# Kernel tuning notes

Hardware: AMD Instinct MI355X
Metric: run time of the kernel (lower is better)

The kernel has to match this reference:

```python
import jax, jax.numpy as jnp
import numpy as np

B, S, E, H, D = 2, 2048, 1024, 16, 64


def setup_inputs() -> dict:
    key = jax.random.key(0)
    ks = jax.random.split(key, 6)
    hidden_states = jax.random.normal(ks[0], (B, S, E), dtype=jnp.float32)
    # causal mask over (SeqLen, KeySeqLen): 1 = attend, 0 = blocked
    mask = jnp.tril(jnp.ones((S, S), dtype=jnp.float32))
    W_attn = jax.random.normal(ks[1], (E, 3, H, D), dtype=jnp.float32) * (E ** -0.5)
    b_attn = jnp.zeros((3, H, D), dtype=jnp.float32)
    W_proj = jax.random.normal(ks[2], (H, D, E), dtype=jnp.float32) * (E ** -0.5)
    b_proj = jnp.zeros((E,), dtype=jnp.float32)
    W_v_ff = jax.random.normal(ks[3], (E, E), dtype=jnp.float32) * (E ** -0.5)
    W_v_gate = jax.random.normal(ks[4], (E, E), dtype=jnp.float32) * (E ** -0.5)
    return {
        "hidden_states": hidden_states,
        "mask": mask,
        "layer_idx": 3,
        "W_attn": W_attn,
        "b_attn": b_attn,
        "W_proj": W_proj,
        "b_proj": b_proj,
        "W_v_ff": W_v_ff,
        "W_v_gate": W_v_gate,
    }


def reference(hidden_states, mask, layer_idx, W_attn, b_attn, W_proj, b_proj, W_v_ff, W_v_gate):
    dtype = hidden_states.dtype
    # c_attn: [B,S,E] -> [B,3,S,H,D]
    qkv = jnp.einsum("bse,eqhd->bqshd", hidden_states, W_attn) + b_attn[:, None, :, :]
    q, k, v = qkv[:, 0], qkv[:, 1], qkv[:, 2]  # [B,S,H,D] (k,v use key-seq axis)

    scale = jax.lax.rsqrt(float(D)) / (layer_idx + 1.0)  # scale_by_inverse_layer_idx
    q = q * scale
    # upcast to fp32 for score computation
    q32 = q.astype(jnp.float32)
    k32 = k.astype(jnp.float32)

    # attention scores: [B,H,S,Skv]
    scores = jnp.einsum("bshd,bthd->bhst", q32, k32)
    scores = scores + (1.0 - mask) * -1e9
    attn_weights = jax.nn.softmax(scores, axis=-1).astype(dtype)
    # dropout is identity (inference=True / p=0)

    # gated V FFN applied over the flattened (H,D) == Embed axis of v
    v_flat = v.reshape(B, S, E)
    v_gate = v_flat @ W_v_gate
    v_ff = v_flat @ W_v_ff
    v_gated = (jax.nn.relu(v_gate) * v_ff).reshape(B, S, H, D)

    # weighted sum over KeySeqLen: [B,S,H,D]
    attn_output = jnp.einsum("bhst,bthd->bshd", attn_weights, v_gated)
    # c_proj: [B,S,H,D] -> [B,S,E]
    out = jnp.einsum("bshd,hde->bse", attn_output, W_proj) + b_proj
    return out
```

## Files before the change

### kernel.cpp

```cpp
#include <hip/hip_runtime.h>
#include <hip/hip_bf16.h>
#include <cstdint>
#include <cstddef>

typedef unsigned short u16;
typedef __bf16 bf16x8 __attribute__((ext_vector_type(8)));
typedef float f32x4 __attribute__((ext_vector_type(4)));

#define LOG2E 1.44269504088896340736f

__device__ __forceinline__ uint32_t f2bf2(float lo, float hi) {
  uint32_t r;
  asm("v_cvt_pk_bf16_f32 %0, %1, %2" : "=v"(r) : "v"(lo), "v"(hi));
  return r;
}
__device__ __forceinline__ u16 f2bf(float f) { return (u16)f2bf2(f, f); }

__device__ __forceinline__ void gload16(const u16* g, u16* l) {
  __builtin_amdgcn_global_load_lds(
      (const __attribute__((address_space(1))) void*)g,
      (__attribute__((address_space(3))) void*)l, 16, 0, 0);
}

__device__ __forceinline__ void xcd_swizzle(int& bx, int& by) {
  const int gx = gridDim.x;
  const int nwg = gx * gridDim.y;
  const int bid = blockIdx.y * gx + blockIdx.x;
  const int s = (bid & 7) * (nwg >> 3) + (bid >> 3);
  bx = s % gx;
  by = s / gx;
}

__global__ __launch_bounds__(256) void transpose_bf16_kernel(
    const float* __restrict__ src, u16* __restrict__ dst, int ld, int c0) {
  __shared__ u16 tile[64][65];
  const int r0 = blockIdx.x * 64, cl0 = blockIdx.y * 64;
  const int tid = threadIdx.x;
#pragma unroll
  for (int i = 0; i < 16; ++i) {
    int idx = i * 256 + tid;
    int r = idx >> 6, c = idx & 63;
    tile[c][r] = f2bf(src[(size_t)(r0 + r) * ld + c0 + cl0 + c]);
  }
  __syncthreads();
#pragma unroll
  for (int i = 0; i < 16; ++i) {
    int idx = i * 256 + tid;
    int c = idx >> 6, r = idx & 63;
    dst[(size_t)(cl0 + c) * 1024 + r0 + r] = tile[c][r];
  }
}

__global__ __launch_bounds__(256) void prep3_kernel(
    const float* __restrict__ Wa, const float* __restrict__ Wg,
    const float* __restrict__ Wf,
    u16* __restrict__ dv, u16* __restrict__ dg, u16* __restrict__ df) {
  __shared__ u16 tile[64][65];
  const int z = blockIdx.z;
  const float* src = (z == 0) ? Wa : (z == 1) ? Wg : Wf;
  u16* dst = (z == 0) ? dv : (z == 1) ? dg : df;
  const int ld = (z == 0) ? 3072 : 1024;
  const int c0 = (z == 0) ? 2048 : 0;
  const int r0 = blockIdx.x * 64, cl0 = blockIdx.y * 64;
  const int tid = threadIdx.x;
#pragma unroll
  for (int i = 0; i < 16; ++i) {
    int idx = i * 256 + tid;
    int r = idx >> 6, c = idx & 63;
    tile[c][r] = f2bf(src[(size_t)(r0 + r) * ld + c0 + cl0 + c]);
  }
  __syncthreads();
#pragma unroll
  for (int i = 0; i < 16; ++i) {
    int idx = i * 256 + tid;
    int c = idx >> 6, r = idx & 63;
    dst[(size_t)(cl0 + c) * 1024 + r0 + r] = tile[c][r];
  }
}

template <int EPI>
__global__ __launch_bounds__(256) void gemm_hA(
    const float* __restrict__ A,
    const u16* __restrict__ Bt,
    u16* __restrict__ O0, u16* __restrict__ O1,
    const float* __restrict__ bias,
    const int* __restrict__ layer_idx) {
  __shared__ u16 lds_a[2][64 * 40];
  __shared__ u16 lds_b[2][128 * 32];
  const int tid = threadIdx.x;
  const int wid = tid >> 6, lane = tid & 63;
  const int lrow = lane & 15, lgrp = lane >> 4;
  int bxs, bys;
  xcd_swizzle(bxs, bys);
  const int brow = bys * 64;
  const int bcol = bxs * 128;
  const int wr = wid >> 1, wc = wid & 1;

  f32x4 acc[2][4] = {};

  const int wchunk0 = wid, wchunk1 = 4 + wid;
  const int cB0 = wchunk0 * 64 + lane, cB1 = wchunk1 * 64 + lane;
  const int rB0 = cB0 >> 2, col8B0 = (cB0 & 3) << 3;
  const int rB1 = cB1 >> 2, col8B1 = (cB1 & 3) << 3;

  gload16(Bt + (size_t)(bcol + rB0) * 1024 + col8B0, lds_b[0] + wchunk0 * 512);
  gload16(Bt + (size_t)(bcol + rB1) * 1024 + col8B1, lds_b[0] + wchunk1 * 512);
  {
    float4 v[2];
#pragma unroll
    for (int j = 0; j < 2; ++j) {
      int idx = j * 256 + tid;
      int m = idx >> 3, k4 = (idx & 7) << 2;
      v[j] = *(const float4*)(A + (size_t)(brow + m) * 1024 + k4);
    }
#pragma unroll
    for (int j = 0; j < 2; ++j) {
      int idx = j * 256 + tid;
      int m = idx >> 3, k4 = (idx & 7) << 2;
      uint2 w;
      w.x = f2bf2(v[j].x, v[j].y);
      w.y = f2bf2(v[j].z, v[j].w);
      *(uint2*)(lds_a[0] + m * 40 + k4) = w;
    }
  }

  for (int k0 = 0; k0 < 1024; k0 += 32) {
    const int bi = (k0 >> 5) & 1;
    __syncthreads();
    bf16x8 af[2], bfr[4];
#pragma unroll
    for (int mi = 0; mi < 2; ++mi)
      af[mi] = *(const bf16x8*)(lds_a[bi] + (wr * 32 + mi * 16 + lrow) * 40 + lgrp * 8);
#pragma unroll
    for (int nj = 0; nj < 4; ++nj)
      bfr[nj] = *(const bf16x8*)(lds_b[bi] + (wc * 64 + nj * 16 + lrow) * 32 + lgrp * 8);

    float4 v[2];
    if (k0 < 992) {
      const int kn = k0 + 32;
      gload16(Bt + (size_t)(bcol + rB0) * 1024 + kn + col8B0, lds_b[bi ^ 1] + wchunk0 * 512);
      gload16(Bt + (size_t)(bcol + rB1) * 1024 + kn + col8B1, lds_b[bi ^ 1] + wchunk1 * 512);
#pragma unroll
      for (int j = 0; j < 2; ++j) {
        int idx = j * 256 + tid;
        int m = idx >> 3, k4 = (idx & 7) << 2;
        v[j] = *(const float4*)(A + (size_t)(brow + m) * 1024 + kn + k4);
      }
    }

#pragma unroll
    for (int mi = 0; mi < 2; ++mi)
#pragma unroll
      for (int nj = 0; nj < 4; ++nj)
        acc[mi][nj] = __builtin_amdgcn_mfma_f32_16x16x32_bf16(af[mi], bfr[nj], acc[mi][nj], 0, 0, 0);

    if (k0 < 992) {
#pragma unroll
      for (int j = 0; j < 2; ++j) {
        int idx = j * 256 + tid;
        int m = idx >> 3, k4 = (idx & 7) << 2;
        uint2 w;
        w.x = f2bf2(v[j].x, v[j].y);
        w.y = f2bf2(v[j].z, v[j].w);
        *(uint2*)(lds_a[bi ^ 1] + m * 40 + k4) = w;
      }
    }
  }

  float scale = 1.0f;
  if (EPI == 0) scale = 0.125f * LOG2E / (1.0f + (float)(*layer_idx));

#pragma unroll
  for (int mi = 0; mi < 2; ++mi) {
#pragma unroll
    for (int nj = 0; nj < 4; ++nj) {
#pragma unroll
      for (int r = 0; r < 4; ++r) {
        int row = brow + wr * 32 + mi * 16 + lgrp * 4 + r;
        int col = bcol + wc * 64 + nj * 16 + lrow;
        float vv = acc[mi][nj][r] + bias[col];
        if (EPI == 0) {
          if (col < 1024) {
            O0[(size_t)row * 1024 + col] = f2bf(vv * scale);
          } else {
            O1[(size_t)row * 1024 + (col - 1024)] = f2bf(vv);
          }
        } else {
          size_t oidx = (size_t)(row >> 11) * 4194304 + (size_t)(row & 2047) * 1024 + col;
          O0[oidx] = f2bf(vv);
        }
      }
    }
  }
}

__global__ __launch_bounds__(256) void gemm_gate(
    const u16* __restrict__ A,
    const u16* __restrict__ Bg, const u16* __restrict__ Bf,
    u16* __restrict__ VgT) {
  __shared__ u16 lds_a[2][64 * 32];
  __shared__ u16 lds_g[2][128 * 32];
  __shared__ u16 lds_f[2][128 * 32];
  const int tid = threadIdx.x;
  const int wid = tid >> 6, lane = tid & 63;
  const int lrow = lane & 15, lgrp = lane >> 4;
  int bxs, bys;
  xcd_swizzle(bxs, bys);
  const int browg = bys * 64;
  const int batch = browg >> 11;
  const int brow = browg & 2047;
  const u16* Ab = A + (size_t)batch * 4194304;
  u16* VgTb = VgT + (size_t)batch * 4194304;
  const int bcol = bxs * 128;
  const int wr = wid >> 1, wc = wid & 1;

  f32x4 accg[2][4] = {};
  f32x4 accf[2][4] = {};

  const int wchunk0 = wid, wchunk1 = 4 + wid;
  const int cA = wchunk0 * 64 + lane;
  const int rA = cA >> 2, col8A = (cA & 3) << 3;
  const int cB0 = wchunk0 * 64 + lane, cB1 = wchunk1 * 64 + lane;
  const int rB0 = cB0 >> 2, col8B0 = (cB0 & 3) << 3;
  const int rB1 = cB1 >> 2, col8B1 = (cB1 & 3) << 3;

  auto stage = [&](int k0, int bi) {
    gload16(Ab + (size_t)(brow + rA) * 1024 + k0 + col8A, lds_a[bi] + wchunk0 * 512);
    gload16(Bg + (size_t)(bcol + rB0) * 1024 + k0 + col8B0, lds_g[bi] + wchunk0 * 512);
    gload16(Bg + (size_t)(bcol + rB1) * 1024 + k0 + col8B1, lds_g[bi] + wchunk1 * 512);
    gload16(Bf + (size_t)(bcol + rB0) * 1024 + k0 + col8B0, lds_f[bi] + wchunk0 * 512);
    gload16(Bf + (size_t)(bcol + rB1) * 1024 + k0 + col8B1, lds_f[bi] + wchunk1 * 512);
  };

  stage(0, 0);
  for (int k0 = 0; k0 < 1024; k0 += 32) {
    const int bi = (k0 >> 5) & 1;
    __syncthreads();
    bf16x8 af[2], bg[4], bff[4];
#pragma unroll
    for (int mi = 0; mi < 2; ++mi)
      af[mi] = *(const bf16x8*)(lds_a[bi] + (wr * 32 + mi * 16 + lrow) * 32 + lgrp * 8);
#pragma unroll
    for (int nj = 0; nj < 4; ++nj) {
      bg[nj]  = *(const bf16x8*)(lds_g[bi] + (wc * 64 + nj * 16 + lrow) * 32 + lgrp * 8);
      bff[nj] = *(const bf16x8*)(lds_f[bi] + (wc * 64 + nj * 16 + lrow) * 32 + lgrp * 8);
    }
    if (k0 < 992) stage(k0 + 32, bi ^ 1);
#pragma unroll
    for (int mi = 0; mi < 2; ++mi)
#pragma unroll
      for (int nj = 0; nj < 4; ++nj) {
        accg[mi][nj] = __builtin_amdgcn_mfma_f32_16x16x32_bf16(af[mi], bg[nj],  accg[mi][nj], 0, 0, 0);
        accf[mi][nj] = __builtin_amdgcn_mfma_f32_16x16x32_bf16(af[mi], bff[nj], accf[mi][nj], 0, 0, 0);
      }
  }

#pragma unroll
  for (int mi = 0; mi < 2; ++mi) {
#pragma unroll
    for (int nj = 0; nj < 4; ++nj) {
      int row0 = brow + wr * 32 + mi * 16 + lgrp * 4;
      int n = bcol + wc * 64 + nj * 16 + lrow;
      int k5 = row0 & 31;
      int s0 = (k5 < 16) ? ((k5 >> 2) * 8) : (((k5 - 16) >> 2) * 8 + 4);
      int pos = (row0 & ~31) + s0;
      uint2 w;
      w.x = f2bf2(fmaxf(accg[mi][nj][0], 0.f) * accf[mi][nj][0],
                  fmaxf(accg[mi][nj][1], 0.f) * accf[mi][nj][1]);
      w.y = f2bf2(fmaxf(accg[mi][nj][2], 0.f) * accf[mi][nj][2],
                  fmaxf(accg[mi][nj][3], 0.f) * accf[mi][nj][3]);
      *(uint2*)(VgTb + (size_t)n * 2048 + pos) = w;
    }
  }
}

__global__ __launch_bounds__(256) void gemm_projf(
    const u16* __restrict__ A,
    const float* __restrict__ Wp,
    float* __restrict__ Cout,
    const float* __restrict__ bias) {
  __shared__ u16 lds_a[2][64 * 32];
  __shared__ u16 lds_bt[2][64 * 40];
  const int tid = threadIdx.x;
  const int wid = tid >> 6, lane = tid & 63;
  const int lrow = lane & 15, lgrp = lane >> 4;
  int bxs, bys;
  xcd_swizzle(bxs, bys);
  const int brow = bys * 64;
  const int bcol = bxs * 64;
  const int wr = wid >> 1, wc = wid & 1;

  f32x4 acc[2][2] = {};

  const int cA = wid * 64 + lane;
  const int rA = cA >> 2, col8A = (cA & 3) << 3;
  const int ng = tid & 15, kp = tid >> 4;
  const int n4 = ng << 2, kk = kp << 1;
  const int kc = kk >> 3, klo = kk & 7;

  auto stageB = [&](int k0, int bi) {
    float4 va = *(const float4*)(Wp + (size_t)(k0 + kk) * 1024 + bcol + n4);
    float4 vb = *(const float4*)(Wp + (size_t)(k0 + kk + 1) * 1024 + bcol + n4);
    const float a4[4] = {va.x, va.y, va.z, va.w};
    const float b4[4] = {vb.x, vb.y, vb.z, vb.w};
#pragma unroll
    for (int i = 0; i < 4; ++i) {
      int row = n4 + i;
      int sw = (kc ^ ((row >> 2) & 3)) << 3;
      u16* p = lds_bt[bi] + row * 40 + sw + klo;
      *(uint32_t*)p = f2bf2(a4[i], b4[i]);
    }
  };

  gload16(A + (size_t)(brow + rA) * 1024 + col8A, lds_a[0] + wid * 512);
  stageB(0, 0);

  for (int k0 = 0; k0 < 1024; k0 += 32) {
    const int bi = (k0 >> 5) & 1;
    __syncthreads();
    bf16x8 af[2], bfr[2];
#pragma unroll
    for (int mi = 0; mi < 2; ++mi)
      af[mi] = *(const bf16x8*)(lds_a[bi] + (wr * 32 + mi * 16 + lrow) * 32 + lgrp * 8);
#pragma unroll
    for (int nj = 0; nj < 2; ++nj) {
      int rowb = wc * 32 + nj * 16 + lrow;
      bfr[nj] = *(const bf16x8*)(lds_bt[bi] + rowb * 40 + ((lgrp ^ ((rowb >> 2) & 3)) << 3));
    }

    if (k0 < 992) {
      const int kn = k0 + 32;
      gload16(A + (size_t)(brow + rA) * 1024 + kn + col8A, lds_a[bi ^ 1] + wid * 512);
      stageB(kn, bi ^ 1);
    }

#pragma unroll
    for (int mi = 0; mi < 2; ++mi)
#pragma unroll
      for (int nj = 0; nj < 2; ++nj)
        acc[mi][nj] = __builtin_amdgcn_mfma_f32_16x16x32_bf16(af[mi], bfr[nj], acc[mi][nj], 0, 0, 0);
  }

#pragma unroll
  for (int mi = 0; mi < 2; ++mi)
#pragma unroll
    for (int nj = 0; nj < 2; ++nj)
#pragma unroll
      for (int r = 0; r < 4; ++r) {
        int row = brow + wr * 32 + mi * 16 + lgrp * 4 + r;
        int col = bcol + wc * 32 + nj * 16 + lrow;
        Cout[(size_t)row * 1024 + col] = acc[mi][nj][r] + bias[col];
      }
}

__global__ __launch_bounds__(256) void attn_kernel(
    const u16* Qb, const u16* __restrict__ Kb,
    const u16* __restrict__ VgTb, u16* AO) {
  __shared__ u16 lds_kv[2][16384];
  __shared__ float lds_ls[4][64];
  const int tid = threadIdx.x, wid = tid >> 6, lane = tid & 63;
  const int lrow = lane & 15, lgrp = lane >> 4;
  const int f = blockIdx.x;
  const int h = f & 15;
  const int idx = f >> 4;
  const int qt = (idx < 16) ? idx : 47 - idx;
  const int nt = (qt >> 1) + 1;

  bf16x8 qf[4][2];
#pragma unroll
  for (int qg = 0; qg < 4; ++qg) {
    const u16* qp = Qb + (size_t)(qt * 64 + qg * 16 + lrow) * 1024 + h * 64 + lgrp * 8;
    qf[qg][0] = *(const bf16x8*)(qp);
    qf[qg][1] = *(const bf16x8*)(qp + 32);
  }

  int krow[4], kch[4], vrow[4], vch[4];
#pragma unroll
  for (int i = 0; i < 4; ++i) {
    int c = i * 256 + tid;
    krow[i] = c >> 3; kch[i] = c & 7;
    vrow[i] = c >> 4; vch[i] = c & 15;
  }
  bf16x8 kreg[4], vreg[4];

  auto stage_load = [&](int t) {
#pragma unroll
    for (int i = 0; i < 4; ++i) {
      kreg[i] = *(const bf16x8*)(Kb + (size_t)(t * 128 + krow[i]) * 1024 + h * 64 + kch[i] * 8);
      vreg[i] = *(const bf16x8*)(VgTb + (size_t)(h * 64 + vrow[i]) * 2048 + t * 128 + vch[i] * 8);
    }
  };
  auto stage_write = [&](int bi) {
#pragma unroll
    for (int i = 0; i < 4; ++i) {
      *(bf16x8*)(lds_kv[bi] + krow[i] * 64 + ((kch[i] ^ (krow[i] & 7)) << 3)) = kreg[i];
      *(bf16x8*)(lds_kv[bi] + 8192 + vrow[i] * 128 + ((vch[i] ^ (vrow[i] & 7)) << 3)) = vreg[i];
    }
  };

  stage_load(0);
  stage_write(0);
  __syncthreads();

  f32x4 oacc[4][4] = {};
  float lsum[4] = {0.f, 0.f, 0.f, 0.f};

  for (int t = 0; t < nt; ++t) {
    const int bi = t & 1;
    if (t + 1 < nt) stage_load(t + 1);
    const u16* lk = lds_kv[bi];
    const u16* lv = lds_kv[bi] + 8192;

    bf16x8 kf[2][2];
#pragma unroll
    for (int ks = 0; ks < 2; ++ks)
#pragma unroll
      for (int nj2 = 0; nj2 < 2; ++nj2) {
        int row = wid * 32 + nj2 * 16 + lrow;
        kf[ks][nj2] = *(const bf16x8*)(lk + row * 64 + (((ks * 4 + lgrp) ^ (lrow & 7)) << 3));
      }
    bf16x8 vf[4];
#pragma unroll
    for (int dt = 0; dt < 4; ++dt)
      vf[dt] = *(const bf16x8*)(lv + (dt * 16 + lrow) * 128 + (((wid * 4 + lgrp) ^ (lrow & 7)) << 3));

    f32x4 sacc[4][2] = {};
#pragma unroll
    for (int qg = 0; qg < 4; ++qg)
#pragma unroll
      for (int ks = 0; ks < 2; ++ks)
#pragma unroll
        for (int nj2 = 0; nj2 < 2; ++nj2)
          sacc[qg][nj2] = __builtin_amdgcn_mfma_f32_16x16x32_bf16(kf[ks][nj2], qf[qg][ks], sacc[qg][nj2], 0, 0, 0);

    const bool last = (t == nt - 1);
#pragma unroll
    for (int qg = 0; qg < 4; ++qg) {
#pragma unroll
      for (int nj2 = 0; nj2 < 2; ++nj2) {
#pragma unroll
        for (int r = 0; r < 4; ++r) {
          float p;
          if (last) {
            int key = t * 128 + wid * 32 + nj2 * 16 + lgrp * 4 + r;
            int srow = qt * 64 + qg * 16 + lrow;
            p = (key > srow) ? 0.f : exp2f(sacc[qg][nj2][r]);
          } else {
            p = exp2f(sacc[qg][nj2][r]);
          }
          sacc[qg][nj2][r] = p;
          lsum[qg] += p;
        }
      }
    }

#pragma unroll
    for (int qg = 0; qg < 4; ++qg) {
      union { uint32_t u[4]; bf16x8 v; } pa;
      pa.u[0] = f2bf2(sacc[qg][0][0], sacc[qg][0][1]);
      pa.u[1] = f2bf2(sacc[qg][0][2], sacc[qg][0][3]);
      pa.u[2] = f2bf2(sacc[qg][1][0], sacc[qg][1][1]);
      pa.u[3] = f2bf2(sacc[qg][1][2], sacc[qg][1][3]);
#pragma unroll
      for (int dt = 0; dt < 4; ++dt)
        oacc[qg][dt] = __builtin_amdgcn_mfma_f32_16x16x32_bf16(pa.v, vf[dt], oacc[qg][dt], 0, 0, 0);
    }

    if (t + 1 < nt) stage_write(bi ^ 1);
    __syncthreads();
  }

#pragma unroll
  for (int qg = 0; qg < 4; ++qg) {
    lsum[qg] += __shfl_xor(lsum[qg], 16);
    lsum[qg] += __shfl_xor(lsum[qg], 32);
  }
  if (lgrp == 0) {
#pragma unroll
    for (int qg = 0; qg < 4; ++qg) lds_ls[wid][qg * 16 + lrow] = lsum[qg];
  }

  float* red = (float*)lds_kv;
#pragma unroll
  for (int qg = 0; qg < 4; ++qg)
#pragma unroll
    for (int dt = 0; dt < 4; ++dt)
      *(f32x4*)(red + dt * 4096 + qg * 1024 + wid * 256 + lane * 4) = oacc[qg][dt];
  __syncthreads();

#pragma unroll
  for (int qg = 0; qg < 4; ++qg) {
    f32x4 s = *(const f32x4*)(red + wid * 4096 + qg * 1024 + 0 * 256 + lane * 4);
#pragma unroll
    for (int w = 1; w < 4; ++w) {
      f32x4 x = *(const f32x4*)(red + wid * 4096 + qg * 1024 + w * 256 + lane * 4);
      s[0] += x[0]; s[1] += x[1]; s[2] += x[2]; s[3] += x[3];
    }
#pragma unroll
    for (int r = 0; r < 4; ++r) {
      int q = qg * 16 + lgrp * 4 + r;
      float ls = lds_ls[0][q] + lds_ls[1][q] + lds_ls[2][q] + lds_ls[3][q];
      AO[(size_t)(qt * 64 + q) * 1024 + h * 64 + wid * 16 + lrow] = f2bf(s[r] / ls);
    }
  }
}

extern "C" void kernel_launch(void* const* d_in, const int* in_sizes, int n_in,
                              void* d_out, int out_size, void* d_ws, size_t ws_size,
                              hipStream_t stream) {
  const float* hidden    = (const float*)d_in[0];
  const int*   layer_idx = (const int*)d_in[2];
  const float* W_attn    = (const float*)d_in[3];
  const float* b_attn    = (const float*)d_in[4];
  const float* W_proj    = (const float*)d_in[5];
  const float* b_proj    = (const float*)d_in[6];
  const float* W_v_ff    = (const float*)d_in[7];
  const float* W_v_gate  = (const float*)d_in[8];

  const size_t MB = 1ull << 20;
  char* ob = (char*)d_out;
  u16* QA = (u16*)(ob);
  u16* QB = (u16*)(ob + 4 * MB);
  u16* QC = (u16*)(ob + 8 * MB);
  u16* QD = (u16*)(ob + 12 * MB);
  u16* WS  = (u16*)d_ws;
  u16* WfT = WS + 1024 * 1024;

  const float* hid0 = hidden;
  const float* hid1 = hidden + (size_t)2048 * 1024;

  prep3_kernel<<<dim3(16, 16, 3), 256, 0, stream>>>(W_attn, W_v_gate, W_v_ff, QD, WS, WfT);
  gemm_hA<1><<<dim3(8, 64), 256, 0, stream>>>(hidden, QD, QA, nullptr, b_attn + 2048, nullptr);
  gemm_gate<<<dim3(8, 64), 256, 0, stream>>>(QA, WS, WfT, QB);
  transpose_bf16_kernel<<<dim3(16, 32), 256, 0, stream>>>(W_attn, QC, 3072, 0);
  gemm_hA<0><<<dim3(16, 32), 256, 0, stream>>>(hid0, QC, WS, QA, b_attn, layer_idx);
  attn_kernel<<<512, 256, 0, stream>>>(WS, QA, QB, WS);
  gemm_hA<0><<<dim3(16, 32), 256, 0, stream>>>(hid1, QC, QA, QB, b_attn, layer_idx);
  attn_kernel<<<512, 256, 0, stream>>>(QA, QB, QD, QA);
  gemm_projf<<<dim3(16, 32), 256, 0, stream>>>(QA, W_proj, (float*)d_out + (size_t)2048 * 1024, b_proj);
  gemm_projf<<<dim3(16, 32), 256, 0, stream>>>(WS, W_proj, (float*)d_out, b_proj);
}
```

Measured before the change: 213.9 us.

## Load K/V attention fragments directly from global into registers, dropping LDS staging

The attention kernel no longer stages K and V tiles through a double-buffered shared-memory array with per-iteration barriers. Each wave now loads its own MFMA operand fragments straight from global memory into two register sets that alternate across iterations, prefetching the next tile while computing the current one. This removes LDS writes and reads and the per-tile __syncthreads, in exchange for uncoalesced, strided global loads (especially the V rows 2048 elements apart) and more live registers.

```diff
diff --git a/kernel.cpp b/kernel.cpp
--- a/kernel.cpp
+++ b/kernel.cpp
@@ -356,7 +356,7 @@
 __global__ __launch_bounds__(256) void attn_kernel(
     const u16* Qb, const u16* __restrict__ Kb,
     const u16* __restrict__ VgTb, u16* AO) {
-  __shared__ u16 lds_kv[2][16384];
+  __shared__ float red[16384];
   __shared__ float lds_ls[4][64];
   const int tid = threadIdx.x, wid = tid >> 6, lane = tid & 63;
   const int lrow = lane & 15, lgrp = lane >> 4;
@@ -374,65 +374,28 @@
     qf[qg][1] = *(const bf16x8*)(qp + 32);
   }
 
-  int krow[4], kch[4], vrow[4], vch[4];
-#pragma unroll
-  for (int i = 0; i < 4; ++i) {
-    int c = i * 256 + tid;
-    krow[i] = c >> 3; kch[i] = c & 7;
-    vrow[i] = c >> 4; vch[i] = c & 15;
-  }
-  bf16x8 kreg[4], vreg[4];
-
-  auto stage_load = [&](int t) {
-#pragma unroll
-    for (int i = 0; i < 4; ++i) {
-      kreg[i] = *(const bf16x8*)(Kb + (size_t)(t * 128 + krow[i]) * 1024 + h * 64 + kch[i] * 8);
-      vreg[i] = *(const bf16x8*)(VgTb + (size_t)(h * 64 + vrow[i]) * 2048 + t * 128 + vch[i] * 8);
-    }
-  };
-  auto stage_write = [&](int bi) {
-#pragma unroll
-    for (int i = 0; i < 4; ++i) {
-      *(bf16x8*)(lds_kv[bi] + krow[i] * 64 + ((kch[i] ^ (krow[i] & 7)) << 3)) = kreg[i];
-      *(bf16x8*)(lds_kv[bi] + 8192 + vrow[i] * 128 + ((vch[i] ^ (vrow[i] & 7)) << 3)) = vreg[i];
-    }
-  };
-
-  stage_load(0);
-  stage_write(0);
-  __syncthreads();
+  const u16* Kh = Kb + h * 64;
+  const u16* Vh = VgTb + (size_t)(h * 64) * 2048;
+  const int krow0 = wid * 32 + lrow;
+  const int kcol = lgrp * 8;
+  const int vcolw = wid * 32 + lgrp * 8;
 
   f32x4 oacc[4][4] = {};
   float lsum[4] = {0.f, 0.f, 0.f, 0.f};
 
-  for (int t = 0; t < nt; ++t) {
-    const int bi = t & 1;
-    if (t + 1 < nt) stage_load(t + 1);
-    const u16* lk = lds_kv[bi];
-    const u16* lv = lds_kv[bi] + 8192;
-
-    bf16x8 kf[2][2];
-#pragma unroll
-    for (int ks = 0; ks < 2; ++ks)
-#pragma unroll
-      for (int nj2 = 0; nj2 < 2; ++nj2) {
-        int row = wid * 32 + nj2 * 16 + lrow;
-        kf[ks][nj2] = *(const bf16x8*)(lk + row * 64 + (((ks * 4 + lgrp) ^ (lrow & 7)) << 3));
-      }
-    bf16x8 vf[4];
-#pragma unroll
-    for (int dt = 0; dt < 4; ++dt)
-      vf[dt] = *(const bf16x8*)(lv + (dt * 16 + lrow) * 128 + (((wid * 4 + lgrp) ^ (lrow & 7)) << 3));
-
+  bf16x8 a00, a10, a01, a11, av0, av1, av2, av3;
+  bf16x8 b00, b10, b01, b11, bv0, bv1, bv2, bv3;
+
+  auto compute = [&](int t, bf16x8& k00, bf16x8& k10, bf16x8& k01, bf16x8& k11,
+                     bf16x8& v0, bf16x8& v1, bf16x8& v2, bf16x8& v3) {
     f32x4 sacc[4][2] = {};
 #pragma unroll
-    for (int qg = 0; qg < 4; ++qg)
-#pragma unroll
-      for (int ks = 0; ks < 2; ++ks)
-#pragma unroll
-        for (int nj2 = 0; nj2 < 2; ++nj2)
-          sacc[qg][nj2] = __builtin_amdgcn_mfma_f32_16x16x32_bf16(kf[ks][nj2], qf[qg][ks], sacc[qg][nj2], 0, 0, 0);
-
+    for (int qg = 0; qg < 4; ++qg) {
+      sacc[qg][0] = __builtin_amdgcn_mfma_f32_16x16x32_bf16(k00, qf[qg][0], sacc[qg][0], 0, 0, 0);
+      sacc[qg][0] = __builtin_amdgcn_mfma_f32_16x16x32_bf16(k10, qf[qg][1], sacc[qg][0], 0, 0, 0);
+      sacc[qg][1] = __builtin_amdgcn_mfma_f32_16x16x32_bf16(k01, qf[qg][0], sacc[qg][1], 0, 0, 0);
+      sacc[qg][1] = __builtin_amdgcn_mfma_f32_16x16x32_bf16(k11, qf[qg][1], sacc[qg][1], 0, 0, 0);
+    }
     const bool last = (t == nt - 1);
 #pragma unroll
     for (int qg = 0; qg < 4; ++qg) {
@@ -453,7 +416,6 @@
         }
       }
     }
-
 #pragma unroll
     for (int qg = 0; qg < 4; ++qg) {
       union { uint32_t u[4]; bf16x8 v; } pa;
@@ -461,13 +423,58 @@
       pa.u[1] = f2bf2(sacc[qg][0][2], sacc[qg][0][3]);
       pa.u[2] = f2bf2(sacc[qg][1][0], sacc[qg][1][1]);
       pa.u[3] = f2bf2(sacc[qg][1][2], sacc[qg][1][3]);
-#pragma unroll
-      for (int dt = 0; dt < 4; ++dt)
-        oacc[qg][dt] = __builtin_amdgcn_mfma_f32_16x16x32_bf16(pa.v, vf[dt], oacc[qg][dt], 0, 0, 0);
-    }
-
-    if (t + 1 < nt) stage_write(bi ^ 1);
-    __syncthreads();
+      oacc[qg][0] = __builtin_amdgcn_mfma_f32_16x16x32_bf16(pa.v, v0, oacc[qg][0], 0, 0, 0);
+      oacc[qg][1] = __builtin_amdgcn_mfma_f32_16x16x32_bf16(pa.v, v1, oacc[qg][1], 0, 0, 0);
+      oacc[qg][2] = __builtin_amdgcn_mfma_f32_16x16x32_bf16(pa.v, v2, oacc[qg][2], 0, 0, 0);
+      oacc[qg][3] = __builtin_amdgcn_mfma_f32_16x16x32_bf16(pa.v, v3, oacc[qg][3], 0, 0, 0);
+    }
+  };
+
+  {
+    const u16* kb = Kh + (size_t)(krow0) * 1024 + kcol;
+    a00 = *(const bf16x8*)(kb);
+    a10 = *(const bf16x8*)(kb + 32);
+    a01 = *(const bf16x8*)(kb + 16 * 1024);
+    a11 = *(const bf16x8*)(kb + 16 * 1024 + 32);
+    const u16* vb = Vh + (size_t)(lrow) * 2048 + vcolw;
+    av0 = *(const bf16x8*)(vb);
+    av1 = *(const bf16x8*)(vb + 16 * 2048);
+    av2 = *(const bf16x8*)(vb + 32 * 2048);
+    av3 = *(const bf16x8*)(vb + 48 * 2048);
+  }
+
+  int t = 0;
+  while (true) {
+    if (t + 1 < nt) {
+      const u16* kb = Kh + (size_t)((t + 1) * 128 + krow0) * 1024 + kcol;
+      b00 = *(const bf16x8*)(kb);
+      b10 = *(const bf16x8*)(kb + 32);
+      b01 = *(const bf16x8*)(kb + 16 * 1024);
+      b11 = *(const bf16x8*)(kb + 16 * 1024 + 32);
+      const u16* vb = Vh + (size_t)(lrow) * 2048 + (t + 1) * 128 + vcolw;
+      bv0 = *(const bf16x8*)(vb);
+      bv1 = *(const bf16x8*)(vb + 16 * 2048);
+      bv2 = *(const bf16x8*)(vb + 32 * 2048);
+      bv3 = *(const bf16x8*)(vb + 48 * 2048);
+    }
+    compute(t, a00, a10, a01, a11, av0, av1, av2, av3);
+    ++t;
+    if (t >= nt) break;
+    if (t + 1 < nt) {
+      const u16* kb = Kh + (size_t)((t + 1) * 128 + krow0) * 1024 + kcol;
+      a00 = *(const bf16x8*)(kb);
+      a10 = *(const bf16x8*)(kb + 32);
+      a01 = *(const bf16x8*)(kb + 16 * 1024);
+      a11 = *(const bf16x8*)(kb + 16 * 1024 + 32);
+      const u16* vb = Vh + (size_t)(lrow) * 2048 + (t + 1) * 128 + vcolw;
+      av0 = *(const bf16x8*)(vb);
+      av1 = *(const bf16x8*)(vb + 16 * 2048);
+      av2 = *(const bf16x8*)(vb + 32 * 2048);
+      av3 = *(const bf16x8*)(vb + 48 * 2048);
+    }
+    compute(t, b00, b10, b01, b11, bv0, bv1, bv2, bv3);
+    ++t;
+    if (t >= nt) break;
   }
 
 #pragma unroll
@@ -480,7 +487,6 @@
     for (int qg = 0; qg < 4; ++qg) lds_ls[wid][qg * 16 + lrow] = lsum[qg];
   }
 
-  float* red = (float*)lds_kv;
 #pragma unroll
   for (int qg = 0; qg < 4; ++qg)
 #pragma unroll
```

Result: slower. 239.1 us (median of 2 runs) (+11.8%).
